# Performance work log

Hardware: AMD Instinct MI355X
Metric: run time of the kernel (lower is better)

## Reference

```python
import jax, jax.numpy as jnp
import numpy as np

ROUTING_ITERS = 3
EPS = 1e-8


def squash(x):
    # scale = ||x||^2 / (1 + ||x||^2); out = scale * x / (||x|| + eps)
    norm = jnp.linalg.norm(x, axis=-1, keepdims=True)
    scale = norm ** 2 / (1.0 + norm ** 2)
    return scale * x / (norm + EPS)


def setup_inputs() -> dict:
    key = jax.random.key(0)
    kx, kw = jax.random.split(key)
    B, R, C, IC, OC = 256, 1152, 10, 8, 16
    x = jax.random.normal(kx, (B, R, IC), dtype=jnp.float32)
    # learned prediction weights: [1, num_routes, num_capsules, in_ch, out_ch]
    weights = jax.random.normal(kw, (1, R, C, IC, OC), dtype=jnp.float32)
    return {"x": x, "weights": weights}


def reference(x, weights):
    # prediction vectors u_hat[b,r,c,o] = sum_i x[b,r,i] * W[r,c,i,o]
    u = jnp.einsum('bri,rcio->brco', x, weights[0])  # [B,R,C,OC]
    b = jnp.zeros(u.shape[:3], dtype=u.dtype)        # routing logits [B,R,C]
    v = jnp.zeros(u.shape[:1] + u.shape[2:], dtype=u.dtype)
    for _ in range(ROUTING_ITERS):
        c = jax.nn.softmax(b, axis=-1)               # coupling coeffs over capsules
        s = jnp.einsum('brc,brco->bco', c, u)        # weighted sum over routes
        v = squash(s)                                # [B,C,OC]
        b = b + jnp.einsum('brco,bco->brc', u, v)    # agreement update
    return v
```

## Files before the change

kernel.cpp:

```cpp
#include <hip/hip_runtime.h>
#include <cstdint>
#include <cstddef>

#define NB 256
#define NR 1152
#define NC 10
#define NI 8
#define NO 16
#define NSPLIT 2
#define NSWEEP 9

static __device__ __forceinline__ uint32_t bf16_pack2(float lo, float hi) {
    uint32_t vl = __float_as_uint(lo);
    vl = vl + 0x7FFFu + ((vl >> 16) & 1u);
    uint32_t vh = __float_as_uint(hi);
    vh = vh + 0x7FFFu + ((vh >> 16) & 1u);
    return (vl >> 16) | (vh & 0xFFFF0000u);
}

__global__ __launch_bounds__(320) void caps_u_kernel(
    const float* __restrict__ x, const float* __restrict__ W,
    uint32_t* __restrict__ u)
{
    const int t  = threadIdx.x;
    const int c  = t >> 5;
    const int rl = (t & 31) >> 2;
    const int oq = t & 3;
    const int rc = blockIdx.x >> 4;
    const int bg = blockIdx.x & 15;
    const int b0 = bg * 16;
    const int r  = rc * 8 + rl;

    __shared__ float xs[16][8][8];

    if (t < 256) {
        const int bi = t >> 4, rem = t & 15;
        const int rr = rem >> 1, hf = rem & 1;
        *(float4*)&xs[bi][rr][hf * 4] =
            *(const float4*)(x + ((size_t)(b0 + bi) * NR + rc * 8 + rr) * 8 + hf * 4);
    }

    const float* wb = W + ((size_t)r * NC + c) * (NI * NO) + oq * 4;
    float4 wf[8];
#pragma unroll
    for (int i = 0; i < 8; ++i) wf[i] = *(const float4*)(wb + i * NO);

    __syncthreads();

    for (int bi = 0; bi < 16; ++bi) {
        const float4 xv4a = *(const float4*)&xs[bi][rl][0];
        const float4 xv4b = *(const float4*)&xs[bi][rl][4];
        const float xr[8] = {xv4a.x, xv4a.y, xv4a.z, xv4a.w,
                             xv4b.x, xv4b.y, xv4b.z, xv4b.w};
        float ax = 0.f, ay = 0.f, az = 0.f, aw = 0.f;
#pragma unroll
        for (int i = 0; i < 8; ++i) {
            const float xv = xr[i];
            ax = fmaf(xv, wf[i].x, ax); ay = fmaf(xv, wf[i].y, ay);
            az = fmaf(xv, wf[i].z, az); aw = fmaf(xv, wf[i].w, aw);
        }
        uint2 s;
        s.x = bf16_pack2(ax, ay);
        s.y = bf16_pack2(az, aw);
        *(uint2*)(u + (((size_t)(b0 + bi) * NC + c) * NR + r) * 8 + oq * 2) = s;
    }
}

__global__ __launch_bounds__(256, 2) void caps_pass_kernel(
    const uint32_t* __restrict__ u, const float* __restrict__ vsum,
    float* __restrict__ part2, const int mode)
{
    const int b  = blockIdx.x >> 1;
    const int sp = blockIdx.x & 1;
    const int t  = threadIdx.x;
    const int oq = t & 3;
    const int rl = t >> 2;

    __shared__ float vss[160];
    __shared__ float sred[4][160];

    if (mode != 0 && t < 160) vss[t] = vsum[(size_t)b * 160 + t];
    __syncthreads();

    float acc[10][4];
#pragma unroll
    for (int c = 0; c < 10; ++c)
#pragma unroll
        for (int j = 0; j < 4; ++j) acc[c][j] = 0.f;

    const uint2* ub = (const uint2*)u + (size_t)b * NC * NR * 4 + oq;

    for (int k = 0; k < NSWEEP; ++k) {
        const int r = sp * (NSWEEP * 64) + k * 64 + rl;
        uint2 q[10];
#pragma unroll
        for (int c = 0; c < 10; ++c) q[c] = ub[((size_t)c * NR + r) * 4];

        if (mode != 0) {
            float lg[10];
#pragma unroll
            for (int c = 0; c < 10; ++c) {
                const float4 vq = *(const float4*)&vss[c * 16 + oq * 4];
                float d = __uint_as_float(q[c].x << 16) * vq.x;
                d = fmaf(__uint_as_float(q[c].x & 0xFFFF0000u), vq.y, d);
                d = fmaf(__uint_as_float(q[c].y << 16),         vq.z, d);
                d = fmaf(__uint_as_float(q[c].y & 0xFFFF0000u), vq.w, d);
                lg[c] = d;
            }
#pragma unroll
            for (int c = 0; c < 10; ++c) {
                lg[c] += __shfl_xor(lg[c], 1);
                lg[c] += __shfl_xor(lg[c], 2);
            }
            float m = lg[0];
#pragma unroll
            for (int c = 1; c < 10; ++c) m = fmaxf(m, lg[c]);
            float wgt[10], ssum = 0.f;
#pragma unroll
            for (int c = 0; c < 10; ++c) { wgt[c] = __expf(lg[c] - m); ssum += wgt[c]; }
            const float inv = 1.f / ssum;
#pragma unroll
            for (int c = 0; c < 10; ++c) {
                const float wv = wgt[c] * inv;
                acc[c][0] = fmaf(wv, __uint_as_float(q[c].x << 16),         acc[c][0]);
                acc[c][1] = fmaf(wv, __uint_as_float(q[c].x & 0xFFFF0000u), acc[c][1]);
                acc[c][2] = fmaf(wv, __uint_as_float(q[c].y << 16),         acc[c][2]);
                acc[c][3] = fmaf(wv, __uint_as_float(q[c].y & 0xFFFF0000u), acc[c][3]);
            }
        } else {
#pragma unroll
            for (int c = 0; c < 10; ++c) {
                acc[c][0] += __uint_as_float(q[c].x << 16);
                acc[c][1] += __uint_as_float(q[c].x & 0xFFFF0000u);
                acc[c][2] += __uint_as_float(q[c].y << 16);
                acc[c][3] += __uint_as_float(q[c].y & 0xFFFF0000u);
            }
        }
    }

#pragma unroll
    for (int off = 4; off <= 32; off <<= 1)
#pragma unroll
        for (int c = 0; c < 10; ++c)
#pragma unroll
            for (int j = 0; j < 4; ++j) acc[c][j] += __shfl_xor(acc[c][j], off);

    const int wv = t >> 6;
    if ((t & 63) < 4) {
#pragma unroll
        for (int c = 0; c < 10; ++c)
#pragma unroll
            for (int j = 0; j < 4; ++j)
                sred[wv][c * 16 + oq * 4 + j] = acc[c][j];
    }
    __syncthreads();

    if (t < 160) {
        float s = sred[0][t] + sred[1][t] + sred[2][t] + sred[3][t];
        if (mode == 0) s *= 0.1f;
        part2[((size_t)sp * NB + b) * 160 + t] = s;
    }
}

__global__ __launch_bounds__(192) void caps_reduce_kernel(
    const float* __restrict__ part2, float* __restrict__ vsum,
    float* __restrict__ out, const int mode)
{
    const int b = blockIdx.x;
    const int t = threadIdx.x;
    if (t >= 160) return;
    float s = 0.f;
#pragma unroll
    for (int sp = 0; sp < NSPLIT; ++sp)
        s += part2[((size_t)sp * NB + b) * 160 + t];
    float n2 = s * s;
    n2 += __shfl_xor(n2, 1);
    n2 += __shfl_xor(n2, 2);
    n2 += __shfl_xor(n2, 4);
    n2 += __shfl_xor(n2, 8);
    const float nrm   = sqrtf(n2);
    const float scale = n2 / (1.f + n2) / (nrm + 1e-8f);
    const float v = scale * s;
    if (mode == 0)      vsum[(size_t)b * 160 + t] = v;
    else if (mode == 1) vsum[(size_t)b * 160 + t] += v;
    else                out[(size_t)b * 160 + t] = v;
}

extern "C" void kernel_launch(void* const* d_in, const int* in_sizes, int n_in,
                              void* d_out, int out_size, void* d_ws, size_t ws_size,
                              hipStream_t stream) {
    const float* x = (const float*)d_in[0];
    const float* W = (const float*)d_in[1];
    float* out = (float*)d_out;

    uint8_t*  ws  = (uint8_t*)d_ws;
    uint32_t* u   = (uint32_t*)ws;
    float*    prt = (float*)(ws + 94371840u);
    float*    vsm = (float*)(ws + 94371840u + 327680u);

    caps_u_kernel     <<<2304, 320, 0, stream>>>(x, W, u);
    caps_pass_kernel  <<<NB * NSPLIT, 256, 0, stream>>>(u, vsm, prt, 0);
    caps_reduce_kernel<<<NB, 192, 0, stream>>>(prt, vsm, nullptr, 0);
    caps_pass_kernel  <<<NB * NSPLIT, 256, 0, stream>>>(u, vsm, prt, 1);
    caps_reduce_kernel<<<NB, 192, 0, stream>>>(prt, vsm, nullptr, 1);
    caps_pass_kernel  <<<NB * NSPLIT, 256, 0, stream>>>(u, vsm, prt, 1);
    caps_reduce_kernel<<<NB, 192, 0, stream>>>(prt, nullptr, out, 2);
}
```

Measured before the change: 155.5 us.

## Fuse first routing iteration's route sum into the prediction kernel

The prediction kernel now also emits per-route-chunk partial sums of u over routes, and a new reduce kernel squashes them, replacing the first full pass over u with uniform coupling. This avoids one full read of the large bf16 u tensor. In exchange it writes and rereads a ~24 MB partial buffer and adds shuffles to the u kernel, plus a launch-bounds/unroll tweak.

```diff
diff --git a/kernel.cpp b/kernel.cpp
--- a/kernel.cpp
+++ b/kernel.cpp
@@ -9,6 +9,7 @@
 #define NO 16
 #define NSPLIT 2
 #define NSWEEP 9
+#define NRC 144
 
 static __device__ __forceinline__ uint32_t bf16_pack2(float lo, float hi) {
     uint32_t vl = __float_as_uint(lo);
@@ -18,9 +19,9 @@
     return (vl >> 16) | (vh & 0xFFFF0000u);
 }
 
-__global__ __launch_bounds__(320) void caps_u_kernel(
+__global__ __launch_bounds__(320, 2) void caps_u_s1_kernel(
     const float* __restrict__ x, const float* __restrict__ W,
-    uint32_t* __restrict__ u)
+    uint32_t* __restrict__ u, float* __restrict__ part1)
 {
     const int t  = threadIdx.x;
     const int c  = t >> 5;
@@ -47,6 +48,7 @@
 
     __syncthreads();
 
+#pragma unroll 2
     for (int bi = 0; bi < 16; ++bi) {
         const float4 xv4a = *(const float4*)&xs[bi][rl][0];
         const float4 xv4b = *(const float4*)&xs[bi][rl][4];
@@ -63,12 +65,50 @@
         s.x = bf16_pack2(ax, ay);
         s.y = bf16_pack2(az, aw);
         *(uint2*)(u + (((size_t)(b0 + bi) * NC + c) * NR + r) * 8 + oq * 2) = s;
-    }
+
+        float sx = ax, sy = ay, sz = az, sw = aw;
+#pragma unroll
+        for (int off = 4; off <= 16; off <<= 1) {
+            sx += __shfl_xor(sx, off); sy += __shfl_xor(sy, off);
+            sz += __shfl_xor(sz, off); sw += __shfl_xor(sw, off);
+        }
+        if ((t & 28) == 0) {
+            const float4 sv = {sx, sy, sz, sw};
+            *(float4*)(part1 + (((size_t)(b0 + bi) * NRC + rc) * 160)
+                       + c * 16 + oq * 4) = sv;
+        }
+    }
+}
+
+__global__ __launch_bounds__(192) void caps_s1_reduce_kernel(
+    const float* __restrict__ part1, float* __restrict__ vsum)
+{
+    const int b = blockIdx.x;
+    const int t = threadIdx.x;
+    if (t >= 160) return;
+    float s0 = 0.f, s1 = 0.f, s2 = 0.f, s3 = 0.f;
+    const float* p = part1 + (size_t)b * NRC * 160 + t;
+#pragma unroll 4
+    for (int g = 0; g < NRC; g += 4) {
+        s0 += p[(g + 0) * 160];
+        s1 += p[(g + 1) * 160];
+        s2 += p[(g + 2) * 160];
+        s3 += p[(g + 3) * 160];
+    }
+    const float s = 0.1f * ((s0 + s1) + (s2 + s3));
+    float n2 = s * s;
+    n2 += __shfl_xor(n2, 1);
+    n2 += __shfl_xor(n2, 2);
+    n2 += __shfl_xor(n2, 4);
+    n2 += __shfl_xor(n2, 8);
+    const float nrm   = sqrtf(n2);
+    const float scale = n2 / (1.f + n2) / (nrm + 1e-8f);
+    vsum[(size_t)b * 160 + t] = scale * s;
 }
 
 __global__ __launch_bounds__(256, 2) void caps_pass_kernel(
     const uint32_t* __restrict__ u, const float* __restrict__ vsum,
-    float* __restrict__ part2, const int mode)
+    float* __restrict__ part2)
 {
     const int b  = blockIdx.x >> 1;
     const int sp = blockIdx.x & 1;
@@ -79,7 +119,7 @@
     __shared__ float vss[160];
     __shared__ float sred[4][160];
 
-    if (mode != 0 && t < 160) vss[t] = vsum[(size_t)b * 160 + t];
+    if (t < 160) vss[t] = vsum[(size_t)b * 160 + t];
     __syncthreads();
 
     float acc[10][4];
@@ -96,45 +136,35 @@
 #pragma unroll
         for (int c = 0; c < 10; ++c) q[c] = ub[((size_t)c * NR + r) * 4];
 
-        if (mode != 0) {
-            float lg[10];
-#pragma unroll
-            for (int c = 0; c < 10; ++c) {
-                const float4 vq = *(const float4*)&vss[c * 16 + oq * 4];
-                float d = __uint_as_float(q[c].x << 16) * vq.x;
-                d = fmaf(__uint_as_float(q[c].x & 0xFFFF0000u), vq.y, d);
-                d = fmaf(__uint_as_float(q[c].y << 16),         vq.z, d);
-                d = fmaf(__uint_as_float(q[c].y & 0xFFFF0000u), vq.w, d);
-                lg[c] = d;
-            }
-#pragma unroll
-            for (int c = 0; c < 10; ++c) {
-                lg[c] += __shfl_xor(lg[c], 1);
-                lg[c] += __shfl_xor(lg[c], 2);
-            }
-            float m = lg[0];
-#pragma unroll
-            for (int c = 1; c < 10; ++c) m = fmaxf(m, lg[c]);
-            float wgt[10], ssum = 0.f;
-#pragma unroll
-            for (int c = 0; c < 10; ++c) { wgt[c] = __expf(lg[c] - m); ssum += wgt[c]; }
-            const float inv = 1.f / ssum;
-#pragma unroll
-            for (int c = 0; c < 10; ++c) {
-                const float wv = wgt[c] * inv;
-                acc[c][0] = fmaf(wv, __uint_as_float(q[c].x << 16),         acc[c][0]);
-                acc[c][1] = fmaf(wv, __uint_as_float(q[c].x & 0xFFFF0000u), acc[c][1]);
-                acc[c][2] = fmaf(wv, __uint_as_float(q[c].y << 16),         acc[c][2]);
-                acc[c][3] = fmaf(wv, __uint_as_float(q[c].y & 0xFFFF0000u), acc[c][3]);
-            }
-        } else {
-#pragma unroll
-            for (int c = 0; c < 10; ++c) {
-                acc[c][0] += __uint_as_float(q[c].x << 16);
-                acc[c][1] += __uint_as_float(q[c].x & 0xFFFF0000u);
-                acc[c][2] += __uint_as_float(q[c].y << 16);
-                acc[c][3] += __uint_as_float(q[c].y & 0xFFFF0000u);
-            }
+        float lg[10];
+#pragma unroll
+        for (int c = 0; c < 10; ++c) {
+            const float4 vq = *(const float4*)&vss[c * 16 + oq * 4];
+            float d = __uint_as_float(q[c].x << 16) * vq.x;
+            d = fmaf(__uint_as_float(q[c].x & 0xFFFF0000u), vq.y, d);
+            d = fmaf(__uint_as_float(q[c].y << 16),         vq.z, d);
+            d = fmaf(__uint_as_float(q[c].y & 0xFFFF0000u), vq.w, d);
+            lg[c] = d;
+        }
+#pragma unroll
+        for (int c = 0; c < 10; ++c) {
+            lg[c] += __shfl_xor(lg[c], 1);
+            lg[c] += __shfl_xor(lg[c], 2);
+        }
+        float m = lg[0];
+#pragma unroll
+        for (int c = 1; c < 10; ++c) m = fmaxf(m, lg[c]);
+        float wgt[10], ssum = 0.f;
+#pragma unroll
+        for (int c = 0; c < 10; ++c) { wgt[c] = __expf(lg[c] - m); ssum += wgt[c]; }
+        const float inv = 1.f / ssum;
+#pragma unroll
+        for (int c = 0; c < 10; ++c) {
+            const float wv = wgt[c] * inv;
+            acc[c][0] = fmaf(wv, __uint_as_float(q[c].x << 16),         acc[c][0]);
+            acc[c][1] = fmaf(wv, __uint_as_float(q[c].x & 0xFFFF0000u), acc[c][1]);
+            acc[c][2] = fmaf(wv, __uint_as_float(q[c].y << 16),         acc[c][2]);
+            acc[c][3] = fmaf(wv, __uint_as_float(q[c].y & 0xFFFF0000u), acc[c][3]);
         }
     }
 
@@ -156,9 +186,8 @@
     __syncthreads();
 
     if (t < 160) {
-        float s = sred[0][t] + sred[1][t] + sred[2][t] + sred[3][t];
-        if (mode == 0) s *= 0.1f;
-        part2[((size_t)sp * NB + b) * 160 + t] = s;
+        part2[((size_t)sp * NB + b) * 160 + t]
+            = sred[0][t] + sred[1][t] + sred[2][t] + sred[3][t];
     }
 }
 
@@ -181,9 +210,8 @@
     const float nrm   = sqrtf(n2);
     const float scale = n2 / (1.f + n2) / (nrm + 1e-8f);
     const float v = scale * s;
-    if (mode == 0)      vsum[(size_t)b * 160 + t] = v;
-    else if (mode == 1) vsum[(size_t)b * 160 + t] += v;
-    else                out[(size_t)b * 160 + t] = v;
+    if (mode == 1) vsum[(size_t)b * 160 + t] += v;
+    else           out[(size_t)b * 160 + t] = v;
 }
 
 extern "C" void kernel_launch(void* const* d_in, const int* in_sizes, int n_in,
@@ -193,16 +221,16 @@
     const float* W = (const float*)d_in[1];
     float* out = (float*)d_out;
 
-    uint8_t*  ws  = (uint8_t*)d_ws;
-    uint32_t* u   = (uint32_t*)ws;
-    float*    prt = (float*)(ws + 94371840u);
-    float*    vsm = (float*)(ws + 94371840u + 327680u);
-
-    caps_u_kernel     <<<2304, 320, 0, stream>>>(x, W, u);
-    caps_pass_kernel  <<<NB * NSPLIT, 256, 0, stream>>>(u, vsm, prt, 0);
-    caps_reduce_kernel<<<NB, 192, 0, stream>>>(prt, vsm, nullptr, 0);
-    caps_pass_kernel  <<<NB * NSPLIT, 256, 0, stream>>>(u, vsm, prt, 1);
-    caps_reduce_kernel<<<NB, 192, 0, stream>>>(prt, vsm, nullptr, 1);
-    caps_pass_kernel  <<<NB * NSPLIT, 256, 0, stream>>>(u, vsm, prt, 1);
-    caps_reduce_kernel<<<NB, 192, 0, stream>>>(prt, nullptr, out, 2);
-}
+    uint8_t*  ws   = (uint8_t*)d_ws;
+    uint32_t* u    = (uint32_t*)ws;
+    float*    prt1 = (float*)(ws + 94371840u);
+    float*    prt2 = (float*)(ws + 94371840u + 23592960u);
+    float*    vsm  = (float*)(ws + 94371840u + 23592960u + 327680u);
+
+    caps_u_s1_kernel     <<<2304, 320, 0, stream>>>(x, W, u, prt1);
+    caps_s1_reduce_kernel<<<NB, 192, 0, stream>>>(prt1, vsm);
+    caps_pass_kernel     <<<NB * NSPLIT, 256, 0, stream>>>(u, vsm, prt2);
+    caps_reduce_kernel   <<<NB, 192, 0, stream>>>(prt2, vsm, nullptr, 1);
+    caps_pass_kernel     <<<NB * NSPLIT, 256, 0, stream>>>(u, vsm, prt2);
+    caps_reduce_kernel   <<<NB, 192, 0, stream>>>(prt2, nullptr, out, 2);
+}
```

Result: faster. 141.6 us (-8.9%).
